# Kernel optimization log

Hardware: AMD Instinct MI355X
Metric: run time of the kernel (lower is better)

## Reference

```python
import jax, jax.numpy as jnp
import numpy as np

B, C_IN, H, W = 8, 256, 32, 32
DK = 256
DV = 256
NH = 8
DKH = DK // NH  # 32
C_OUT = 512
KS, PAD = 3, 1


def setup_inputs() -> dict:
    key = jax.random.key(0)
    ks = jax.random.split(key, 9)
    s = 0.05
    return {
        "x": jax.random.normal(ks[0], (B, C_IN, H, W), jnp.float32),
        "w_qkv": jax.random.normal(ks[1], (2 * DK + DV, C_IN, 1, 1), jnp.float32) * s,
        "b_qkv": jnp.zeros((2 * DK + DV,), jnp.float32),
        "w_attn": jax.random.normal(ks[2], (DV, DV, 1, 1), jnp.float32) * s,
        "b_attn": jnp.zeros((DV,), jnp.float32),
        "w_out": jax.random.normal(ks[3], (C_OUT - DV, C_IN, KS, KS), jnp.float32) * s,
        "b_out": jnp.zeros((C_OUT - DV,), jnp.float32),
        # torch init: dkh**-0.5 + rand
        "key_rel_w": DKH ** (-0.5) + jax.random.uniform(ks[4], (2 * W - 1, DKH), jnp.float32),
        "key_rel_h": DKH ** (-0.5) + jax.random.uniform(ks[5], (2 * H - 1, DKH), jnp.float32),
    }


def conv2d(x, w, b, pad):
    y = jax.lax.conv_general_dilated(
        x, w, window_strides=(1, 1), padding=[(pad, pad), (pad, pad)],
        dimension_numbers=("NCHW", "OIHW", "NCHW"))
    return y + b[None, :, None, None]


def rel_to_abs(x):
    # x: [b, nh, L, 2L-1] -> [b, nh, L, L] (skew trick)
    b, nh, L, _ = x.shape
    x = jnp.pad(x, ((0, 0), (0, 0), (0, 0), (0, 1)))
    flat = x.reshape(b, nh, L * 2 * L)
    flat = jnp.pad(flat, ((0, 0), (0, 0), (0, L - 1)))
    final = flat.reshape(b, nh, L + 1, 2 * L - 1)
    return final[:, :, :L, L - 1:]


def relative_logits_1d(q, rel_k, Hd, Wd, transpose_mask):
    # q: [B, NH, DKH, Hd, Wd]; rel_k: [2*Wd-1, DKH]
    rel = jnp.einsum("bhdxy,md->bhxym", q, rel_k)          # [B,NH,Hd,Wd,2Wd-1]
    rel = rel.reshape(-1, NH * Hd, Wd, 2 * Wd - 1)
    rel = rel_to_abs(rel)                                   # [B,NH*Hd,Wd,Wd]
    rel = rel.reshape(-1, NH, Hd, 1, Wd, Wd)
    rel = jnp.broadcast_to(rel, (rel.shape[0], NH, Hd, Hd, Wd, Wd))
    rel = jnp.transpose(rel, transpose_mask)
    return rel.reshape(-1, NH, Hd * Wd, Hd * Wd)


def reference(x, w_qkv, b_qkv, w_attn, b_attn, w_out, b_out, key_rel_w, key_rel_h):
    conv_out = conv2d(x, w_out, b_out, PAD)                 # [B, C_OUT-DV, H, W]
    qkv = conv2d(x, w_qkv, b_qkv, 0)                        # [B, 2DK+DV, H, W]
    q, k, v = jnp.split(qkv, [DK, 2 * DK], axis=1)
    q = q.reshape(B, NH, DKH, H * W) * (DKH ** -0.5)        # scaled BEFORE rel logits (as in torch)
    k = k.reshape(B, NH, DKH, H * W)
    v = v.reshape(B, NH, DV // NH, H * W)
    logits = jnp.einsum("bhdl,bhdm->bhlm", q, k)            # [B,NH,HW,HW]
    q5 = q.reshape(B, NH, DKH, H, W)
    w_rel = relative_logits_1d(q5, key_rel_w, H, W, (0, 1, 2, 4, 3, 5))
    h_rel = relative_logits_1d(jnp.transpose(q5, (0, 1, 2, 4, 3)), key_rel_h, W, H, (0, 1, 4, 2, 5, 3))
    logits = logits + h_rel + w_rel
    weights = jax.nn.softmax(logits, axis=-1)
    attn = jnp.einsum("bhlm,bhdm->bhdl", weights, v)        # [B,NH,DVH,HW]
    attn = attn.reshape(B, DV, H, W)
    attn = conv2d(attn, w_attn, b_attn, 0)
    return jnp.concatenate([conv_out, attn], axis=1)        # [B, C_OUT, H, W]
```

## Files before the change

kernel.cpp:

```cpp
#include <hip/hip_runtime.h>
#include <hip/hip_bf16.h>


typedef __hip_bfloat16 bf16;
typedef __attribute__((ext_vector_type(8))) short bf16x8;
typedef __attribute__((ext_vector_type(4))) float f32x4;

__device__ __forceinline__ float blo(unsigned int v) { return __uint_as_float(v << 16); }
__device__ __forceinline__ float bhi(unsigned int v) { return __uint_as_float(v & 0xffff0000u); }
__device__ __forceinline__ unsigned short f2bfbits(float f) {
  union { bf16 h; unsigned short u; } cv; cv.h = __float2bfloat16(f); return cv.u;
}
__device__ __forceinline__ unsigned int cvt_pk_bf16(float lo, float hi) {
  unsigned int r;
  asm("v_cvt_pk_bf16_f32 %0, %1, %2" : "=v"(r) : "v"(lo), "v"(hi));
  return r;
}
__device__ __forceinline__ float exp2_f(float x) {
#if __has_builtin(__builtin_amdgcn_exp2f)
  return __builtin_amdgcn_exp2f(x);
#else
  return exp2f(x);
#endif
}

__global__ __launch_bounds__(256) void prep_kernel(
    const float* __restrict__ x, const float* __restrict__ wout,
    bf16* __restrict__ xT, bf16* __restrict__ wob0, bf16* __restrict__ wob1)
{
  int bid = blockIdx.x, tid = threadIdx.x;
  if (bid < 2048) {
    __shared__ float t[32 * 33];
    int b = bid >> 8, rem = bid & 255;
    int ci0 = (rem >> 5) * 32, l0 = (rem & 31) * 32;
    {
      int ciL = tid >> 3, lL4 = (tid & 7) * 4;
      float4 v = *(const float4*)(x + (size_t)(b * 256 + ci0 + ciL) * 1024 + l0 + lL4);
      t[ciL * 33 + lL4 + 0] = v.x; t[ciL * 33 + lL4 + 1] = v.y;
      t[ciL * 33 + lL4 + 2] = v.z; t[ciL * 33 + lL4 + 3] = v.w;
    }
    __syncthreads();
    {
      int lL = tid >> 3, cS = (tid & 7) * 4;
      unsigned int p0 = (unsigned int)f2bfbits(t[(cS + 0) * 33 + lL]) |
                        ((unsigned int)f2bfbits(t[(cS + 1) * 33 + lL]) << 16);
      unsigned int p1 = (unsigned int)f2bfbits(t[(cS + 2) * 33 + lL]) |
                        ((unsigned int)f2bfbits(t[(cS + 3) * 33 + lL]) << 16);
      uint2 u2; u2.x = p0; u2.y = p1;
      *(uint2*)(xT + ((size_t)(b * 1024) + l0 + lL) * 256 + ci0 + cS) = u2;
    }
  } else {
    int t0 = (bid - 2048) * 256 + tid;
#pragma unroll
    for (int s = 0; s < 8; ++s) {
      int u = s * 9216 + t0;
      int chunkblk = u / 2304;
      int within = u - chunkblk * 2304;
      int co63 = within / 36;
      int r = within - co63 * 36;
      int kidx = r >> 2, cig = r & 3;
      int co = (chunkblk >> 3) * 64 + co63;
      int ci = (chunkblk & 7) * 32 + cig * 8;
      union { unsigned short h[8]; uint4 u4; } pk;
#pragma unroll
      for (int j = 0; j < 8; ++j)
        pk.h[j] = f2bfbits(wout[(size_t)(co * 256 + ci + j) * 9 + kidx]);
      bf16* dst = (chunkblk < 28) ? (wob0 + (size_t)chunkblk * 18432)
                                  : (wob1 + (size_t)(chunkblk - 28) * 18432);
      *(uint4*)(dst + (size_t)within * 8) = pk.u4;
    }
  }
}

__global__ __launch_bounds__(256) void convqkv_kernel(
    const bf16* __restrict__ xT,
    const bf16* __restrict__ wob0, const bf16* __restrict__ wob1,
    const float* __restrict__ b_out, float* __restrict__ out,
    const float* __restrict__ wq, const float* __restrict__ b_qkv,
    bf16* __restrict__ qT, bf16* __restrict__ kR, bf16* __restrict__ vW)
{
  __shared__ __align__(16) short smem[27104];
  int tid = threadIdx.x, lane = tid & 63, wave = tid >> 6;
  int m16 = lane & 15, quad = lane >> 4;

  if (blockIdx.x < 256) {
    short* wS = smem;
    short* xS = smem + 18944;
    int bid = blockIdx.x;
    int rc = bid & 7, cotile = (bid >> 3) & 3, b = bid >> 5;
    int y0 = rc * 4;

    f32x4 acc[8];
#pragma unroll
    for (int t = 0; t < 8; ++t) acc[t] = (f32x4){0.f, 0.f, 0.f, 0.f};

    for (int ck = 0; ck < 8; ++ck) {
      __syncthreads();
      int cb = cotile * 8 + ck;
      const bf16* wbase = (cb < 28) ? (wob0 + (size_t)cb * 18432)
                                    : (wob1 + (size_t)(cb - 28) * 18432);
#pragma unroll
      for (int r = 0; r < 9; ++r) {
        int u = r * 256 + tid;
        *(uint4*)(wS + (u / 36) * 296 + (u % 36) * 8) = *(const uint4*)(wbase + (size_t)u * 8);
      }
#pragma unroll
      for (int r = 0; r < 3; ++r) {
        int u = r * 256 + tid;
        int pos = u >> 2, seg = u & 3;
        int row = pos >> 5, col = pos & 31;
        int gy = y0 - 1 + row;
        uint4 val = make_uint4(0u, 0u, 0u, 0u);
        if (gy >= 0 && gy < 32)
          val = *(const uint4*)(xT + ((size_t)(b * 1024) + gy * 32 + col) * 256 + ck * 32 + seg * 8);
        *(uint4*)(xS + (row * 34 + col + 1) * 40 + seg * 8) = val;
      }
      if (tid < 48) {
        int pos = tid >> 2, seg = tid & 3;
        int row = pos >> 1, side = pos & 1;
        *(uint4*)(xS + (row * 34 + side * 33) * 40 + seg * 8) = make_uint4(0u, 0u, 0u, 0u);
      }
      __syncthreads();
#pragma unroll
      for (int kidx = 0; kidx < 9; ++kidx) {
        int dy = kidx / 3, dx = kidx - dy * 3;
        bf16x8 af = *(const bf16x8*)(wS + (wave * 16 + m16) * 296 + kidx * 32 + quad * 8);
#pragma unroll
        for (int t = 0; t < 8; ++t) {
          int row = (t >> 1) + dy;
          int col = (t & 1) * 16 + m16 + dx;
          bf16x8 bf = *(const bf16x8*)(xS + (row * 34 + col) * 40 + quad * 8);
          acc[t] = __builtin_amdgcn_mfma_f32_16x16x32_bf16(af, bf, acc[t], 0, 0, 0);
        }
      }
    }

    int cob = cotile * 64 + wave * 16 + quad * 4;
#pragma unroll
    for (int i = 0; i < 4; ++i) {
      float bv = b_out[cob + i];
#pragma unroll
      for (int t = 0; t < 8; ++t) {
        int y = y0 + (t >> 1), xc = (t & 1) * 16 + m16;
        out[((size_t)(b * 512) + cob + i) * 1024 + y * 32 + xc] = acc[t][i] + bv;
      }
    }
  } else {
    short* aS = smem;
    short* bS = smem + 4608;
    int bid2 = blockIdx.x - 256;
    int ltile = bid2 & 7;
    int rest = bid2 >> 3;
    int ctile = rest % 12;
    int b = rest / 12;
    int l0 = ltile * 128;
    int cbase = ctile * 64;

    f32x4 acc[8];
#pragma unroll
    for (int t = 0; t < 8; ++t) acc[t] = (f32x4){0.f, 0.f, 0.f, 0.f};

    for (int ck = 0; ck < 4; ++ck) {
      __syncthreads();
#pragma unroll
      for (int r = 0; r < 4; ++r) {
        int u = r * 256 + tid;
        int c = u >> 4, s4 = u & 15;
        float4 v = *(const float4*)(wq + (size_t)(cbase + c) * 256 + ck * 64 + s4 * 4);
        unsigned int p0 = (unsigned int)f2bfbits(v.x) | ((unsigned int)f2bfbits(v.y) << 16);
        unsigned int p1 = (unsigned int)f2bfbits(v.z) | ((unsigned int)f2bfbits(v.w) << 16);
        uint2 u2; u2.x = p0; u2.y = p1;
        *(uint2*)(aS + c * 72 + s4 * 4) = u2;
      }
#pragma unroll
      for (int r = 0; r < 4; ++r) {
        int u = r * 256 + tid;
        int l = u >> 3, seg = u & 7;
        *(uint4*)(bS + l * 72 + seg * 8) =
            *(const uint4*)(xT + ((size_t)(b * 1024) + l0 + l) * 256 + ck * 64 + seg * 8);
      }
      __syncthreads();
#pragma unroll
      for (int ks = 0; ks < 2; ++ks) {
        bf16x8 af = *(const bf16x8*)(aS + (wave * 16 + m16) * 72 + ks * 32 + quad * 8);
#pragma unroll
        for (int t = 0; t < 8; ++t) {
          bf16x8 bf = *(const bf16x8*)(bS + (t * 16 + m16) * 72 + ks * 32 + quad * 8);
          acc[t] = __builtin_amdgcn_mfma_f32_16x16x32_bf16(af, bf, acc[t], 0, 0, 0);
        }
      }
    }

    __syncthreads();
    short* ldsT = smem + wave * 3072;
    int cb = cbase + wave * 16;
    bool isq = (ctile < 4);
    float bv[4];
#pragma unroll
    for (int i = 0; i < 4; ++i) bv[i] = b_qkv[cb + quad * 4 + i];
#pragma unroll
    for (int t = 0; t < 8; ++t) {
#pragma unroll
      for (int i = 0; i < 4; ++i) {
        float v = acc[t][i] + bv[i];
        if (isq) v *= 0.17677669529663689f;
        ldsT[(t * 16 + m16) * 24 + quad * 4 + i] = (short)f2bfbits(v);
      }
    }
    if (ctile < 8) {
      bf16* dst = isq ? qT : kR;
      int coff = isq ? cb : cb - 256;
#pragma unroll
      for (int rep = 0; rep < 4; ++rep) {
        int u = rep * 64 + lane;
        int l = u >> 1, half = u & 1;
        int c0 = coff + half * 8;
        int head = b * 8 + (c0 >> 5), d0 = c0 & 31;
        *(uint4*)(dst + ((size_t)head * 1024 + l0 + l) * 32 + d0) =
            *(const uint4*)(ldsT + l * 24 + half * 8);
      }
    } else {
      int dcol = lane >> 2, lg = lane & 3;
      int c2 = (cb - 512) + dcol;
      int head = b * 8 + (c2 >> 5), gd = c2 & 31;
      int dt = gd >> 4, m16v = gd & 15;
      int cch = ltile * 2 + (lg >> 1);
      int ksv = lg & 1;
      bf16* vbase = vW + (size_t)head * 32768 + cch * 2048 + (dt * 2 + ksv) * 512 + m16v * 8;
#pragma unroll
      for (int s = 0; s < 4; ++s) {
#pragma unroll
        for (int p = 0; p < 4; ++p) {
          int j0 = lg * 32 + s * 8 + p * 2;
          unsigned int u0 = (unsigned short)ldsT[j0 * 24 + dcol];
          unsigned int u1 = (unsigned short)ldsT[(j0 + 1) * 24 + dcol];
          unsigned int w = u0 | (u1 << 16);
          int quadp = (s & 1) * 2 + (p >> 1);
          int jj = (p & 1) * 2 + (s >> 1) * 4;
          *(unsigned int*)(vbase + quadp * 128 + jj) = w;
        }
      }
    }
  }
}

__global__ __launch_bounds__(128) void attn_mfma_kernel(
    const bf16* __restrict__ qT, const bf16* __restrict__ kR, const bf16* __restrict__ vW,
    const float* __restrict__ krw, const float* __restrict__ krh,
    bf16* __restrict__ attL)
{
  __shared__ __align__(16) char smem[34816];
  float* RWf = (float*)smem;
  float* RHf = (float*)(smem + 17408);

  const float L2E = 1.4426950408889634f;

  int tid = threadIdx.x;
  int lane = tid & 63, wave = tid >> 6;
  int m16 = lane & 15, quad = lane >> 4;
  int bid = blockIdx.x;
  int head = ((bid & 7) << 3) | ((bid >> 3) & 7);
  int qt = bid >> 6;
  int row0 = qt * 64;
  int b = head >> 3, h = head & 7;

#pragma unroll
  for (int mt = 0; mt < 2; ++mt) {
    int mtile = wave * 2 + mt;
    int mrow = mtile * 16 + m16;
    bool valid = (mrow < 63);
    float4 w0 = make_float4(0.f, 0.f, 0.f, 0.f), w1 = w0, h0 = w0, h1 = w0;
    if (valid) {
      w0 = *(const float4*)(krw + mrow * 32 + quad * 8);
      w1 = *(const float4*)(krw + mrow * 32 + quad * 8 + 4);
      h0 = *(const float4*)(krh + mrow * 32 + quad * 8);
      h1 = *(const float4*)(krh + mrow * 32 + quad * 8 + 4);
    }
    union { unsigned int w[4]; bf16x8 v; } aw, ah;
    aw.w[0] = cvt_pk_bf16(w0.x * L2E, w0.y * L2E);
    aw.w[1] = cvt_pk_bf16(w0.z * L2E, w0.w * L2E);
    aw.w[2] = cvt_pk_bf16(w1.x * L2E, w1.y * L2E);
    aw.w[3] = cvt_pk_bf16(w1.z * L2E, w1.w * L2E);
    ah.w[0] = cvt_pk_bf16(h0.x * L2E, h0.y * L2E);
    ah.w[1] = cvt_pk_bf16(h0.z * L2E, h0.w * L2E);
    ah.w[2] = cvt_pk_bf16(h1.x * L2E, h1.y * L2E);
    ah.w[3] = cvt_pk_bf16(h1.z * L2E, h1.w * L2E);
#pragma unroll
    for (int nt = 0; nt < 4; ++nt) {
      bf16x8 qf = *(const bf16x8*)(
          qT + ((size_t)head * 1024 + row0 + nt * 16 + m16) * 32 + quad * 8);
      f32x4 z = (f32x4){0.f, 0.f, 0.f, 0.f};
      f32x4 dw = __builtin_amdgcn_mfma_f32_16x16x32_bf16(aw.v, qf, z, 0, 0, 0);
      f32x4 dh = __builtin_amdgcn_mfma_f32_16x16x32_bf16(ah.v, qf, z, 0, 0, 0);
#pragma unroll
      for (int i = 0; i < 4; ++i) {
        int mr = mtile * 16 + quad * 4 + i;
        RWf[mr * 68 + nt * 16 + m16] = dw[i];
        RHf[mr * 68 + nt * 16 + m16] = dh[i];
      }
    }
  }
  __syncthreads();

  bf16x8 afrag[2];
  float rwreg[2][2][4];
  int qloc0 = wave * 32 + m16;
#pragma unroll
  for (int sub = 0; sub < 2; ++sub) {
    int qloc = qloc0 + sub * 16;
    afrag[sub] = *(const bf16x8*)(
        qT + ((size_t)head * 1024 + row0 + qloc) * 32 + quad * 8);
    int qm = qloc & 31;
#pragma unroll
    for (int par = 0; par < 2; ++par)
#pragma unroll
      for (int i = 0; i < 4; ++i)
        rwreg[sub][par][i] = RWf[(par * 16 + quad * 4 + i - qm + 31) * 68 + qloc];
  }
  int qy = qt * 2 + wave;
  const float* rhp0 = RHf + (31 - qy) * 68 + qloc0;
  const float* rhp1 = rhp0 + 16;

  const bf16* kp = kR + (size_t)head * 32768 + m16 * 32 + quad * 8;
  const bf16* vp = vW + (size_t)head * 32768 + lane * 8;

  f32x4 oacc[2][2];
#pragma unroll
  for (int sub = 0; sub < 2; ++sub) {
    oacc[sub][0] = (f32x4){0.f, 0.f, 0.f, 0.f};
    oacc[sub][1] = (f32x4){0.f, 0.f, 0.f, 0.f};
  }
  float rsp[2] = {0.f, 0.f};

#pragma unroll 1
  for (int c = 0; c < 16; ++c) {
    union { uint4 u; bf16x8 v; } kf[4], vf[4];
#pragma unroll
    for (int t = 0; t < 4; ++t)
      kf[t].u = *(const uint4*)(kp + c * 2048 + t * 512);
#pragma unroll
    for (int q = 0; q < 4; ++q)
      vf[q].u = *(const uint4*)(vp + c * 2048 + q * 512);

    float rh[2][2];
    rh[0][0] = rhp0[(c * 2 + 0) * 68];  rh[0][1] = rhp0[(c * 2 + 1) * 68];
    rh[1][0] = rhp1[(c * 2 + 0) * 68];  rh[1][1] = rhp1[(c * 2 + 1) * 68];

    f32x4 sacc[2][4];
#pragma unroll
    for (int t = 0; t < 4; ++t) {
      f32x4 z = (f32x4){0.f, 0.f, 0.f, 0.f};
#pragma unroll
      for (int sub = 0; sub < 2; ++sub)
        sacc[sub][t] = __builtin_amdgcn_mfma_f32_16x16x32_bf16(kf[t].v, afrag[sub], z, 0, 0, 0);
    }

    unsigned int pk[2][4][2];
#pragma unroll
    for (int sub = 0; sub < 2; ++sub) {
#pragma unroll
      for (int t = 0; t < 4; ++t) {
        float rhv = rh[sub][t >> 1];
        float e0 = exp2_f(fmaf(sacc[sub][t][0], L2E, rwreg[sub][t & 1][0] + rhv));
        float e1 = exp2_f(fmaf(sacc[sub][t][1], L2E, rwreg[sub][t & 1][1] + rhv));
        float e2 = exp2_f(fmaf(sacc[sub][t][2], L2E, rwreg[sub][t & 1][2] + rhv));
        float e3 = exp2_f(fmaf(sacc[sub][t][3], L2E, rwreg[sub][t & 1][3] + rhv));
        rsp[sub] += (e0 + e1) + (e2 + e3);
        pk[sub][t][0] = cvt_pk_bf16(e0, e1);
        pk[sub][t][1] = cvt_pk_bf16(e2, e3);
      }
    }

#pragma unroll
    for (int ks = 0; ks < 2; ++ks) {
#pragma unroll
      for (int sub = 0; sub < 2; ++sub) {
        union { unsigned int w[4]; bf16x8 v; } pf;
        pf.w[0] = pk[sub][2 * ks][0];     pf.w[1] = pk[sub][2 * ks][1];
        pf.w[2] = pk[sub][2 * ks + 1][0]; pf.w[3] = pk[sub][2 * ks + 1][1];
#pragma unroll
        for (int dt = 0; dt < 2; ++dt) {
          oacc[sub][dt] = __builtin_amdgcn_mfma_f32_16x16x32_bf16(
              vf[dt * 2 + ks].v, pf.v, oacc[sub][dt], 0, 0, 0);
        }
      }
    }
  }

#pragma unroll
  for (int sub = 0; sub < 2; ++sub) {
    rsp[sub] += __shfl_xor(rsp[sub], 16, 64);
    rsp[sub] += __shfl_xor(rsp[sub], 32, 64);
    float invs = 1.0f / rsp[sub];
    int grow = row0 + qloc0 + sub * 16;
#pragma unroll
    for (int dt = 0; dt < 2; ++dt) {
      uint2 st;
      st.x = cvt_pk_bf16(oacc[sub][dt][0] * invs, oacc[sub][dt][1] * invs);
      st.y = cvt_pk_bf16(oacc[sub][dt][2] * invs, oacc[sub][dt][3] * invs);
      *(uint2*)(attL + ((size_t)b * 1024 + grow) * 256 + h * 32 + dt * 16 + quad * 4) = st;
    }
  }
}

__global__ __launch_bounds__(256) void attnout_mfma_kernel(
    const bf16* __restrict__ attL, const float* __restrict__ w, const float* __restrict__ bias,
    float* __restrict__ out)
{
  __shared__ __align__(16) short smem[13824];
  short* aS = smem;
  short* bS = smem + 4608;

  int tid = threadIdx.x, lane = tid & 63, wave = tid >> 6;
  int m16 = lane & 15, quad = lane >> 4;
  int l0 = blockIdx.x * 128;
  int cotile = blockIdx.y;
  int b = blockIdx.z;
  int cbase = cotile * 64;

  f32x4 acc[8];
#pragma unroll
  for (int t = 0; t < 8; ++t) acc[t] = (f32x4){0.f, 0.f, 0.f, 0.f};

  for (int ck = 0; ck < 4; ++ck) {
    __syncthreads();
#pragma unroll
    for (int r = 0; r < 4; ++r) {
      int u = r * 256 + tid;
      int c = u >> 4, s4 = u & 15;
      float4 v = *(const float4*)(w + (size_t)(cbase + c) * 256 + ck * 64 + s4 * 4);
      unsigned int p0 = (unsigned int)f2bfbits(v.x) | ((unsigned int)f2bfbits(v.y) << 16);
      unsigned int p1 = (unsigned int)f2bfbits(v.z) | ((unsigned int)f2bfbits(v.w) << 16);
      uint2 u2; u2.x = p0; u2.y = p1;
      *(uint2*)(aS + c * 72 + s4 * 4) = u2;
    }
#pragma unroll
    for (int r = 0; r < 4; ++r) {
      int u = r * 256 + tid;
      int l = u >> 3, seg = u & 7;
      *(uint4*)(bS + l * 72 + seg * 8) =
          *(const uint4*)(attL + ((size_t)(b * 1024) + l0 + l) * 256 + ck * 64 + seg * 8);
    }
    __syncthreads();
#pragma unroll
    for (int ks = 0; ks < 2; ++ks) {
      bf16x8 af = *(const bf16x8*)(aS + (wave * 16 + m16) * 72 + ks * 32 + quad * 8);
#pragma unroll
      for (int t = 0; t < 8; ++t) {
        bf16x8 bf = *(const bf16x8*)(bS + (t * 16 + m16) * 72 + ks * 32 + quad * 8);
        acc[t] = __builtin_amdgcn_mfma_f32_16x16x32_bf16(af, bf, acc[t], 0, 0, 0);
      }
    }
  }

  int co = cbase + wave * 16 + quad * 4;
#pragma unroll
  for (int i = 0; i < 4; ++i) {
    float bv = bias[co + i];
    size_t obase = ((size_t)(b * 512) + 256 + co + i) * 1024 + l0;
#pragma unroll
    for (int t = 0; t < 8; ++t)
      out[obase + t * 16 + m16] = acc[t][i] + bv;
  }
}

extern "C" void kernel_launch(void* const* d_in, const int* in_sizes, int n_in,
                              void* d_out, int out_size, void* d_ws, size_t ws_size,
                              hipStream_t stream) {
  const float* x      = (const float*)d_in[0];
  const float* w_qkv  = (const float*)d_in[1];
  const float* b_qkv  = (const float*)d_in[2];
  const float* w_attn = (const float*)d_in[3];
  const float* b_attn = (const float*)d_in[4];
  const float* w_out  = (const float*)d_in[5];
  const float* b_out  = (const float*)d_in[6];
  const float* krw    = (const float*)d_in[7];
  const float* krh    = (const float*)d_in[8];
  float* out = (float*)d_out;

  bf16* ws    = (bf16*)d_ws;
  bf16* xT    = ws;
  bf16* attL  = ws;
  bf16* qT    = ws + 2097152;
  bf16* kR    = ws + 4194304;
  bf16* vF    = ws + 6291456;

  bf16* wob0 = (bf16*)(out + (size_t)(0 * 512 + 256) * 1024);
  bf16* wob1 = (bf16*)(out + (size_t)(1 * 512 + 256) * 1024);

  prep_kernel<<<dim3(2084), 256, 0, stream>>>(x, w_out, xT, wob0, wob1);
  convqkv_kernel<<<dim3(1024), 256, 0, stream>>>(xT, wob0, wob1, b_out, out,
                                                 w_qkv, b_qkv, qT, kR, vF);
  attn_mfma_kernel<<<dim3(1024), 128, 0, stream>>>(qT, kR, vF, krw, krh, attL);
  attnout_mfma_kernel<<<dim3(8, 4, 8), 256, 0, stream>>>(attL, w_attn, b_attn, out);
}
```

Measured before the change: 138.5 us.

## Split attention key range across two wave groups with LDS reduction

The attention kernel grows from 128 to 256 threads. Each pair of waves handles half of the 16 key chunks, and partial output accumulators and row sums are merged through shared memory before normalisation. The relative-logit table setup is spread over four waves, one tile each. The aim is more parallelism per block and a shorter serial key loop, at the cost of extra barriers and LDS traffic for the reduction. Since no max subtraction is used, summing partial exponential sums stays valid.

```diff
diff --git a/kernel.cpp b/kernel.cpp
--- a/kernel.cpp
+++ b/kernel.cpp
@@ -244,7 +244,7 @@
   }
 }
 
-__global__ __launch_bounds__(128) void attn_mfma_kernel(
+__global__ __launch_bounds__(256) void attn_mfma_kernel(
     const bf16* __restrict__ qT, const bf16* __restrict__ kR, const bf16* __restrict__ vW,
     const float* __restrict__ krw, const float* __restrict__ krh,
     bf16* __restrict__ attL)
@@ -252,11 +252,14 @@
   __shared__ __align__(16) char smem[34816];
   float* RWf = (float*)smem;
   float* RHf = (float*)(smem + 17408);
+  float* pO  = (float*)smem;
+  float* pR  = (float*)(smem + 8192);
 
   const float L2E = 1.4426950408889634f;
 
   int tid = threadIdx.x;
   int lane = tid & 63, wave = tid >> 6;
+  int qw = wave & 1, kw = wave >> 1;
   int m16 = lane & 15, quad = lane >> 4;
   int bid = blockIdx.x;
   int head = ((bid & 7) << 3) | ((bid >> 3) & 7);
@@ -264,9 +267,8 @@
   int row0 = qt * 64;
   int b = head >> 3, h = head & 7;
 
-#pragma unroll
-  for (int mt = 0; mt < 2; ++mt) {
-    int mtile = wave * 2 + mt;
+  {
+    int mtile = wave;
     int mrow = mtile * 16 + m16;
     bool valid = (mrow < 63);
     float4 w0 = make_float4(0.f, 0.f, 0.f, 0.f), w1 = w0, h0 = w0, h1 = w0;
@@ -304,7 +306,7 @@
 
   bf16x8 afrag[2];
   float rwreg[2][2][4];
-  int qloc0 = wave * 32 + m16;
+  int qloc0 = qw * 32 + m16;
 #pragma unroll
   for (int sub = 0; sub < 2; ++sub) {
     int qloc = qloc0 + sub * 16;
@@ -317,7 +319,9 @@
       for (int i = 0; i < 4; ++i)
         rwreg[sub][par][i] = RWf[(par * 16 + quad * 4 + i - qm + 31) * 68 + qloc];
   }
-  int qy = qt * 2 + wave;
+  __syncthreads();
+
+  int qy = qt * 2 + qw;
   const float* rhp0 = RHf + (31 - qy) * 68 + qloc0;
   const float* rhp1 = rhp0 + 16;
 
@@ -332,8 +336,9 @@
   }
   float rsp[2] = {0.f, 0.f};
 
+  int c0 = kw * 8;
 #pragma unroll 1
-  for (int c = 0; c < 16; ++c) {
+  for (int c = c0; c < c0 + 8; ++c) {
     union { uint4 u; bf16x8 v; } kf[4], vf[4];
 #pragma unroll
     for (int t = 0; t < 4; ++t)
@@ -387,18 +392,42 @@
     }
   }
 
-#pragma unroll
-  for (int sub = 0; sub < 2; ++sub) {
-    rsp[sub] += __shfl_xor(rsp[sub], 16, 64);
-    rsp[sub] += __shfl_xor(rsp[sub], 32, 64);
-    float invs = 1.0f / rsp[sub];
-    int grow = row0 + qloc0 + sub * 16;
-#pragma unroll
-    for (int dt = 0; dt < 2; ++dt) {
-      uint2 st;
-      st.x = cvt_pk_bf16(oacc[sub][dt][0] * invs, oacc[sub][dt][1] * invs);
-      st.y = cvt_pk_bf16(oacc[sub][dt][2] * invs, oacc[sub][dt][3] * invs);
-      *(uint2*)(attL + ((size_t)b * 1024 + grow) * 256 + h * 32 + dt * 16 + quad * 4) = st;
+  if (kw == 1) {
+#pragma unroll
+    for (int sub = 0; sub < 2; ++sub) {
+#pragma unroll
+      for (int dt = 0; dt < 2; ++dt)
+#pragma unroll
+        for (int i = 0; i < 4; ++i)
+          pO[(((sub * 2 + dt) * 4 + i) * 128) + qw * 64 + lane] = oacc[sub][dt][i];
+      pR[sub * 128 + qw * 64 + lane] = rsp[sub];
+    }
+  }
+  __syncthreads();
+  if (kw == 0) {
+#pragma unroll
+    for (int sub = 0; sub < 2; ++sub) {
+#pragma unroll
+      for (int dt = 0; dt < 2; ++dt)
+#pragma unroll
+        for (int i = 0; i < 4; ++i)
+          oacc[sub][dt][i] += pO[(((sub * 2 + dt) * 4 + i) * 128) + qw * 64 + lane];
+      rsp[sub] += pR[sub * 128 + qw * 64 + lane];
+    }
+
+#pragma unroll
+    for (int sub = 0; sub < 2; ++sub) {
+      rsp[sub] += __shfl_xor(rsp[sub], 16, 64);
+      rsp[sub] += __shfl_xor(rsp[sub], 32, 64);
+      float invs = 1.0f / rsp[sub];
+      int grow = row0 + qloc0 + sub * 16;
+#pragma unroll
+      for (int dt = 0; dt < 2; ++dt) {
+        uint2 st;
+        st.x = cvt_pk_bf16(oacc[sub][dt][0] * invs, oacc[sub][dt][1] * invs);
+        st.y = cvt_pk_bf16(oacc[sub][dt][2] * invs, oacc[sub][dt][3] * invs);
+        *(uint2*)(attL + ((size_t)b * 1024 + grow) * 256 + h * 32 + dt * 16 + quad * 4) = st;
+      }
     }
   }
 }
@@ -491,6 +520,6 @@
   prep_kernel<<<dim3(2084), 256, 0, stream>>>(x, w_out, xT, wob0, wob1);
   convqkv_kernel<<<dim3(1024), 256, 0, stream>>>(xT, wob0, wob1, b_out, out,
                                                  w_qkv, b_qkv, qT, kR, vF);
-  attn_mfma_kernel<<<dim3(1024), 128, 0, stream>>>(qT, kR, vF, krw, krh, attL);
+  attn_mfma_kernel<<<dim3(1024), 256, 0, stream>>>(qT, kR, vF, krw, krh, attL);
   attnout_mfma_kernel<<<dim3(8, 4, 8), 256, 0, stream>>>(attL, w_attn, b_attn, out);
 }
```

Result: no change. 139.4 us (+0.6%).
